# Kernel tuning notes

Hardware: AMD Instinct MI355X
Metric: run time of the kernel (lower is better)

Reference implementation:

```python
import jax, jax.numpy as jnp
import numpy as np
from jax import lax


def setup_inputs() -> dict:
    key = jax.random.key(0)
    ks = jax.random.split(key, 12)
    B, T = 64, 256
    H, EN, ET, D = 512, 256, 256, 256  # hidden, embN, embT, embT_dyn (==ET since embedding_sizeT_dyn=None)
    VN, VT, VS = 300, 1000, 100       # vocab_sizeN, vocab_sizeT, num static ids (static_x_ids = range(100))
    s = 0.05
    ar = jnp.arange(VT)
    inp = {}
    inp["n_input"] = jax.random.randint(ks[0], (B, T), 0, VN)
    inp["t_input"] = jax.random.randint(ks[1], (B, T), 0, VT)
    inp["is_static_vocab"] = ar < VS                      # membership test (t in static_x_ids)
    inp["static2dense"] = jnp.where(ar < VS, ar, 0)       # static id -> row in embeddingT
    inp["dynamic2dense"] = jnp.where(ar >= VS, ar - VS, 0)  # dynamic id -> dense dynamic slot
    inp["embN"] = jax.random.normal(ks[2], (VN, EN)) * s
    inp["embT"] = jax.random.normal(ks[3], (VS, ET)) * s
    inp["W_ih"] = jax.random.normal(ks[4], (4 * H, EN + ET)) * s
    inp["W_hh"] = jax.random.normal(ks[5], (4 * H, H)) * s
    inp["b_ih"] = jax.random.normal(ks[6], (4 * H,)) * s
    inp["b_hh"] = jax.random.normal(ks[7], (4 * H,)) * s
    inp["Wd_ih"] = jax.random.normal(ks[8], (4 * D, EN + H)) * s
    inp["Wd_hh"] = jax.random.normal(ks[9], (4 * D, D)) * s
    inp["bd_ih"] = jax.random.normal(ks[10], (4 * D,)) * s
    inp["bd_hh"] = jax.random.normal(ks[11], (4 * D,)) * s
    inp["hid_init"] = jnp.zeros((H,))
    inp["cell_init"] = jnp.zeros((H,))
    inp["dyn_init_h"] = jnp.zeros((1, D))  # anonym_type='pure_zeros'
    inp["dyn_init_c"] = jnp.zeros((1, D))
    return inp


def _lstm_cell(x, h, c, Wi, Wh, bi, bh):
    # torch.nn.LSTMCell gate order: i, f, g, o
    g = x @ Wi.T + bi + h @ Wh.T + bh
    i, f, gg, o = jnp.split(g, 4, axis=-1)
    c2 = jax.nn.sigmoid(f) * c + jax.nn.sigmoid(i) * jnp.tanh(gg)
    return jax.nn.sigmoid(o) * jnp.tanh(c2), c2


def reference(n_input, t_input, is_static_vocab, static2dense, dynamic2dense,
              embN, embT, W_ih, W_hh, b_ih, b_hh,
              Wd_ih, Wd_hh, bd_ih, bd_hh,
              hid_init, cell_init, dyn_init_h, dyn_init_c):
    # The torch module's growing (lookup_table, de_h, de_c) cache is equivalent to
    # per-(batch, dynamic-token) state arrays Hd/Cd [B, V_dyn, D] with a 'seen' flag:
    # each (b, token) pair owns exactly one cache slot that is read/updated in place.
    B, T = n_input.shape
    H = hid_init.shape[0]
    D = dyn_init_h.shape[-1]
    VD = int(dynamic2dense.max()) + 1  # number of dynamic vocab slots (static at setup)
    bidx = jnp.arange(B)
    init_h = jnp.broadcast_to(dyn_init_h, (B, D))
    init_c = jnp.broadcast_to(dyn_init_c, (B, D))

    def step(carry, xt):
        h, c, seen, Hd, Cd = carry
        nt, tt = xt
        is_st = is_static_vocab[tt]            # [B] bool
        didx = dynamic2dense[tt]               # [B] dynamic slot (garbage 0 for static rows, masked below)
        sn = seen[bidx, didx]                  # was this (b, token) created before?
        hd_prev = jnp.where(sn[:, None], Hd[bidx, didx], init_h)
        cd_prev = jnp.where(sn[:, None], Cd[bidx, didx], init_c)
        n_emb = embN[nt]                       # [B, EN] (dropout=0 -> plain lookup)
        # emb_transform is identity (embedding_sizeT_dyn is None)
        h_tensor = jnp.where(is_st[:, None], embT[static2dense[tt]], hd_prev)  # [B, ET]
        h_new, c_new = _lstm_cell(jnp.concatenate([n_emb, h_tensor], 1), h, c, W_ih, W_hh, b_ih, b_hh)
        # dynamic-embedding LSTM: input is (n_emb, previous main hidden h)
        hd_new, cd_new = _lstm_cell(jnp.concatenate([n_emb, h], 1), hd_prev, cd_prev, Wd_ih, Wd_hh, bd_ih, bd_hh)
        dyn = (~is_st)[:, None]
        Hd = Hd.at[bidx, didx].set(jnp.where(dyn, hd_new, Hd[bidx, didx]))
        Cd = Cd.at[bidx, didx].set(jnp.where(dyn, cd_new, Cd[bidx, didx]))
        seen = seen.at[bidx, didx].set(sn | (~is_st))
        return (h_new, c_new, seen, Hd, Cd), h_new

    h0 = jnp.broadcast_to(hid_init, (B, H)) + 0.0
    c0 = jnp.broadcast_to(cell_init, (B, H)) + 0.0
    carry0 = (h0, c0,
              jnp.zeros((B, VD), dtype=bool),
              jnp.zeros((B, VD, D), dtype=embN.dtype),
              jnp.zeros((B, VD, D), dtype=embN.dtype))
    _, outs = lax.scan(step, carry0, (n_input.T, t_input.T))  # outs: [T, B, H]
    return jnp.transpose(outs, (1, 0, 2))                     # [B, T, H]
```

## Files before the change

### kernel.cpp

```cpp
#include <hip/hip_runtime.h>


typedef _Float16 f16;
typedef _Float16 f16x8 __attribute__((ext_vector_type(8)));
typedef float f32x4 __attribute__((ext_vector_type(4)));

#define B_ 64
#define T_ 256
#define H_ 512
#define EN_ 256
#define ET_ 256
#define D_ 256
#define VN_ 300
#define VS_ 100

#define NB_MAIN_ 128
#define NB_DYN_ 64
#define NBLK_ 192
#define NTHR_ 256
#define NSH_ 64
#define PER_SHARD_ (NBLK_ / NSH_)
#define POLL_CAP_ (1u << 22)

static constexpr size_t OFF_CNT  = 0;
static constexpr size_t OFF_EMBN = 4096;
static constexpr size_t OFF_EMBT = OFF_EMBN + (size_t)VN_ * EN_ * 2;
static constexpr size_t OFF_DINH = OFF_EMBT + (size_t)VS_ * ET_ * 2;
static constexpr size_t OFF_PREV = OFF_DINH + 1024;
static constexpr size_t OFF_HH   = OFF_PREV + (size_t)T_ * B_ * 4;
static constexpr size_t OFF_HD   = OFF_HH + (size_t)(T_ + 1) * B_ * H_ * 2;
static constexpr size_t OFF_CD   = OFF_HD + (size_t)T_ * B_ * D_ * 2;
static constexpr size_t WS_NEED  = OFF_CD + (size_t)T_ * B_ * D_ * 4;

struct RnnParams {
  const int* n_input; const int* t_input; const int* s2d;
  const float* W_ih; const float* W_hh; const float* b_ih; const float* b_hh;
  const float* Wd_ih; const float* Wd_hh; const float* bd_ih; const float* bd_hh;
  const float* cell_init; const float* dyn_init_c;
  const f16* embN16; const f16* embT16; const f16* dynih16;
  const int* prev;
  f16* Hhist; f16* HdHist; float* CdHist;
  float* out; unsigned* cnt;
};

__device__ __forceinline__ float sigm(float x) { return 1.f / (1.f + __expf(-x)); }
__device__ __forceinline__ float tanh_fast(float x) {
  float e = __expf(2.f * x);
  return 1.f - 2.f / (e + 1.f);
}

__device__ __forceinline__ void cstore8(void* p, unsigned long long v) {
  __hip_atomic_store((unsigned long long*)p, v, __ATOMIC_RELAXED,
                     __HIP_MEMORY_SCOPE_AGENT);
}
__device__ __forceinline__ void cstore16(void* p, f32x4 v) {
  asm volatile("global_store_dwordx4 %0, %1, off sc0 sc1"
               :: "v"(p), "v"(v) : "memory");
}
__device__ __forceinline__ float4 scload16f(const float* p) {
  float4 v;
  asm volatile("global_load_dwordx4 %0, %1, off sc0 sc1\n\ts_waitcnt vmcnt(0)"
               : "=&v"(v) : "v"(p) : "memory");
  return v;
}
__device__ __forceinline__ void lds_barrier() {
  asm volatile("s_waitcnt lgkmcnt(0)\n\ts_barrier" ::: "memory");
}

__global__ void setup_kernel(const float* embN, const float* embT,
                             const float* hid_init, const float* dyn_init_h,
                             f16* embN16, f16* embT16, f16* dynih16,
                             f16* Hhist0, unsigned* cnt) {
  int i = blockIdx.x * blockDim.x + threadIdx.x;
  if (i < 1024)      cnt[i] = 0u;
  if (i < VN_ * EN_) embN16[i] = (f16)embN[i];
  if (i < VS_ * ET_) embT16[i] = (f16)embT[i];
  if (i < D_)        dynih16[i] = (f16)dyn_init_h[i];
  if (i < B_ * H_) {
    int b = i >> 9, k = i & 511;
    Hhist0[(k >> 3) * 512 + b * 8 + (k & 7)] = (f16)hid_init[k];
  }
  __threadfence();
}

__global__ void prev_kernel(const int* t_input, const int* s2d, int* prev) {
  int idx = blockIdx.x * blockDim.x + threadIdx.x;
  if (idx < B_ * T_) {
    int b = idx / T_, t = idx % T_;
    int tt = t_input[b * T_ + t];
    int p = -1;
    if (s2d[tt] != tt) {
      for (int q = t - 1; q >= 0; --q)
        if (t_input[b * T_ + q] == tt) { p = q; break; }
    }
    prev[t * B_ + b] = p;
  }
  __threadfence();
}

__device__ __forceinline__ void resolve(const RnnParams& p, bool isDyn, int t, int b,
                                        int tprev,
                                        const f16** aN, const f16** aX,
                                        const float** aC, int* dynw, int* rc) {
  const int nt = p.n_input[b * T_ + t];
  aN[b] = p.embN16 + (size_t)nt * EN_;
  const int tt = p.t_input[b * T_ + t];
  const int pv = p.prev[t * B_ + b];
  rc[b] = (pv >= 0 && pv == tprev) ? 1 : 0;
  const f16* hd = (pv >= 0) ? (p.HdHist + ((size_t)pv * B_ + b) * D_) : p.dynih16;
  const int s2 = p.s2d[tt];
  const bool st = (s2 == tt);
  if (!isDyn) {
    aX[b] = st ? (p.embT16 + (size_t)s2 * ET_) : hd;
  } else {
    aX[b] = hd;
    aC[b] = (pv >= 0) ? (p.CdHist + ((size_t)pv * B_ + b) * D_) : p.dyn_init_c;
    dynw[b] = st ? 0 : 1;
  }
}

__global__ __launch_bounds__(NTHR_, 1) void rnn_main(RnnParams p) {
  const int blk  = blockIdx.x;
  const int tid  = threadIdx.x;
  const int wave = tid >> 6;
  const int lane = tid & 63;
  const bool isDyn = (blk >= NB_MAIN_);
  const int u0 = isDyn ? (blk - NB_MAIN_) * 4 : blk * 4;

  __threadfence();

  __shared__ float s_bias[16];
  __shared__ float s_scr[64][17];
  __shared__ const f16*  s_aN[2][64];
  __shared__ const f16*  s_aX[2][64];
  __shared__ const float* s_aC[2][64];
  __shared__ int s_dynw[2][64];
  __shared__ int s_rc[2][64];

  const int nIdx = lane & 15;
  const int ui = nIdx & 3, gate = nIdx >> 2;
  const int ko = (lane >> 4) * 8;
  f16x8 w[32];
  if (!isDyn) {
    const int r = gate * H_ + u0 + ui;
#pragma unroll
    for (int s = 0; s < 32; ++s) {
      const int k = s * 32 + ko;
      const float* src = (k < 512) ? (p.W_ih + (size_t)r * 512 + k)
                                   : (p.W_hh + (size_t)r * 512 + (k - 512));
      f16x8 v;
#pragma unroll
      for (int j = 0; j < 8; ++j) v[j] = (f16)src[j];
      w[s] = v;
    }
  } else {
    const int r = gate * D_ + u0 + ui;
#pragma unroll
    for (int s = 0; s < 32; ++s) {
      const int k = s * 32 + ko;
      const float* src = (k < 768) ? (p.Wd_ih + (size_t)r * 768 + k)
                                   : (p.Wd_hh + (size_t)r * 256 + (k - 768));
      f16x8 v;
#pragma unroll
      for (int j = 0; j < 8; ++j) v[j] = (f16)src[j];
      w[s] = v;
    }
  }
  if (tid < 16) {
    int g2 = tid >> 2, un2 = tid & 3;
    s_bias[tid] = isDyn ? (p.bd_ih[g2 * D_ + u0 + un2] + p.bd_hh[g2 * D_ + u0 + un2])
                        : (p.b_ih[g2 * H_ + u0 + un2] + p.b_hh[g2 * H_ + u0 + un2]);
  }
  float creg[4] = {0.f, 0.f, 0.f, 0.f};
  if (tid < 64 && !isDyn) {
#pragma unroll
    for (int un = 0; un < 4; ++un) creg[un] = p.cell_init[u0 + un];
  }
  if (tid < 64)
    resolve(p, isDyn, 0, tid, -1, s_aN[0], s_aX[0], s_aC[0], s_dynw[0], s_rc[0]);
  __syncthreads();

  const int b = (wave << 4) + (lane & 15);
  f16x8 pf[16];
  float4 cvp = {0.f, 0.f, 0.f, 0.f};
  {
    const f16* pN = s_aN[0][b];
    const f16* pX = s_aX[0][b];
#pragma unroll
    for (int i = 0; i < 8; ++i) pf[i] = *(const f16x8*)(pN + i * 32 + ko);
#pragma unroll
    for (int i = 0; i < 8; ++i) pf[8 + i] = *(const f16x8*)(pX + i * 32 + ko);
    if (isDyn && tid < 64) cvp = *(const float4*)(s_aC[0][tid] + u0);
  }
  const int hoff = ((lane >> 4) << 9) + ((lane & 15) << 3) + (wave << 7);

  for (int t = 0; t < T_; ++t) {
    const int pb = t & 1;

    const f16* pH2 = p.Hhist + (size_t)t * 32768 + hoff;
    f16x8 hh[16];
#pragma unroll
    for (int i = 0; i < 16; ++i) hh[i] = *(const f16x8*)(pH2 + i * 2048);

    {
      const int need = s_rc[pb][b];
      if (__any(need)) {
        if (need) {
          const f16* pX = s_aX[pb][b];
#pragma unroll
          for (int i = 0; i < 8; ++i)
            asm volatile("global_load_dwordx4 %0, %1, off sc0 sc1"
                         : "=&v"(pf[8 + i]) : "v"(pX + i * 32 + ko));
        }
        asm volatile("s_waitcnt vmcnt(0)" ::: "memory");
        __builtin_amdgcn_sched_barrier(0);
      }
    }

    f32x4 ac[4] = {{0,0,0,0},{0,0,0,0},{0,0,0,0},{0,0,0,0}};
    if (!isDyn) {
#pragma unroll
      for (int i = 0; i < 8; ++i)
        ac[i & 3] = __builtin_amdgcn_mfma_f32_16x16x32_f16(pf[i], w[i], ac[i & 3], 0, 0, 0);
#pragma unroll
      for (int i = 0; i < 8; ++i)
        ac[i & 3] = __builtin_amdgcn_mfma_f32_16x16x32_f16(pf[8 + i], w[8 + i], ac[i & 3], 0, 0, 0);
#pragma unroll
      for (int i = 0; i < 16; ++i)
        ac[i & 3] = __builtin_amdgcn_mfma_f32_16x16x32_f16(hh[i], w[16 + i], ac[i & 3], 0, 0, 0);
    } else {
#pragma unroll
      for (int i = 0; i < 8; ++i)
        ac[i & 3] = __builtin_amdgcn_mfma_f32_16x16x32_f16(pf[i], w[i], ac[i & 3], 0, 0, 0);
#pragma unroll
      for (int i = 0; i < 8; ++i)
        ac[i & 3] = __builtin_amdgcn_mfma_f32_16x16x32_f16(pf[8 + i], w[24 + i], ac[i & 3], 0, 0, 0);
#pragma unroll
      for (int i = 0; i < 16; ++i)
        ac[i & 3] = __builtin_amdgcn_mfma_f32_16x16x32_f16(hh[i], w[8 + i], ac[i & 3], 0, 0, 0);
    }
    f32x4 acc = (ac[0] + ac[1]) + (ac[2] + ac[3]);
#pragma unroll
    for (int j = 0; j < 4; ++j)
      s_scr[(wave << 4) + ((lane >> 4) << 2) + j][lane & 15] = acc[j];
    lds_barrier();

    if (tid < 64) {
      const int eb = tid;
      if (isDyn) {
        const int cneed = s_rc[pb][eb];
        if (__any(cneed)) {
          if (cneed) cvp = scload16f(s_aC[pb][eb] + u0);
          __builtin_amdgcn_sched_barrier(0);
        }
      }
      float g[16];
#pragma unroll
      for (int n = 0; n < 16; ++n) g[n] = s_scr[eb][n] + s_bias[n];
      if (!isDyn) {
        float4 ho;
        union { f16 h[4]; unsigned long long u; } pk;
#pragma unroll
        for (int un = 0; un < 4; ++un) {
          float c = sigm(g[4 + un]) * creg[un] + sigm(g[un]) * tanh_fast(g[8 + un]);
          creg[un] = c;
          float h = sigm(g[12 + un]) * tanh_fast(c);
          (&ho.x)[un] = h;
          pk.h[un] = (f16)h;
        }
        *(float4*)&p.out[((size_t)eb * T_ + t) * H_ + u0] = ho;
        cstore8(&p.Hhist[(size_t)(t + 1) * 32768 + (size_t)(u0 >> 3) * 512
                         + (size_t)eb * 8 + ((u0 >> 2) & 1) * 4], pk.u);
      } else {
        const float cold[4] = {cvp.x, cvp.y, cvp.z, cvp.w};
        f32x4 co;
        union { f16 h[4]; unsigned long long u; } pk;
#pragma unroll
        for (int un = 0; un < 4; ++un) {
          float c = sigm(g[4 + un]) * cold[un] + sigm(g[un]) * tanh_fast(g[8 + un]);
          float h = sigm(g[12 + un]) * tanh_fast(c);
          pk.h[un] = (f16)h;
          co[un] = c;
        }
        if (s_dynw[pb][eb]) {
          cstore8(&p.HdHist[((size_t)t * B_ + eb) * D_ + u0], pk.u);
          cstore16(&p.CdHist[((size_t)t * B_ + eb) * D_ + u0], co);
        }
      }
    } else if (tid < 128 && t + 1 < T_) {
      resolve(p, isDyn, t + 1, tid - 64, t,
              s_aN[pb ^ 1], s_aX[pb ^ 1], s_aC[pb ^ 1], s_dynw[pb ^ 1], s_rc[pb ^ 1]);
    }
    lds_barrier();

    if (t + 1 < T_) {
      if (wave == 0) {
        asm volatile("s_waitcnt vmcnt(0)" ::: "memory");
        if (tid == 0)
          __hip_atomic_fetch_add(&p.cnt[(blk & (NSH_ - 1)) << 4], 1u,
                                 __ATOMIC_RELAXED, __HIP_MEMORY_SCOPE_AGENT);
      }
      {
        const f16* pN2 = s_aN[pb ^ 1][b];
        const f16* pX2 = s_aX[pb ^ 1][b];
#pragma unroll
        for (int i = 0; i < 8; ++i) pf[i] = *(const f16x8*)(pN2 + i * 32 + ko);
#pragma unroll
        for (int i = 0; i < 8; ++i) pf[8 + i] = *(const f16x8*)(pX2 + i * 32 + ko);
        if (isDyn && tid < 64) cvp = *(const float4*)(s_aC[pb ^ 1][tid] + u0);
      }
      if (wave == 1) {
        const unsigned tgt = (unsigned)(t + 1) * PER_SHARD_;
        unsigned it = 0;
        while (__hip_atomic_load(&p.cnt[lane << 4], __ATOMIC_RELAXED,
                                 __HIP_MEMORY_SCOPE_AGENT) < tgt &&
               ++it < POLL_CAP_)
          __builtin_amdgcn_s_sleep(1);
      }
      lds_barrier();
    }
  }
}

extern "C" void kernel_launch(void* const* d_in, const int* in_sizes, int n_in,
                              void* d_out, int out_size, void* d_ws, size_t ws_size,
                              hipStream_t stream) {
  (void)in_sizes; (void)n_in; (void)out_size;
  const int* n_input   = (const int*)d_in[0];
  const int* t_input   = (const int*)d_in[1];
  const int* s2d       = (const int*)d_in[3];
  const float* embN    = (const float*)d_in[5];
  const float* embT    = (const float*)d_in[6];
  const float* W_ih    = (const float*)d_in[7];
  const float* W_hh    = (const float*)d_in[8];
  const float* b_ih    = (const float*)d_in[9];
  const float* b_hh    = (const float*)d_in[10];
  const float* Wd_ih   = (const float*)d_in[11];
  const float* Wd_hh   = (const float*)d_in[12];
  const float* bd_ih   = (const float*)d_in[13];
  const float* bd_hh   = (const float*)d_in[14];
  const float* hid_init  = (const float*)d_in[15];
  const float* cell_init = (const float*)d_in[16];
  const float* dyn_init_h = (const float*)d_in[17];
  const float* dyn_init_c = (const float*)d_in[18];

  char* ws = (char*)d_ws;
  unsigned* cnt  = (unsigned*)(ws + OFF_CNT);
  f16* embN16    = (f16*)(ws + OFF_EMBN);
  f16* embT16    = (f16*)(ws + OFF_EMBT);
  f16* dynih16   = (f16*)(ws + OFF_DINH);
  int* prev      = (int*)(ws + OFF_PREV);
  f16* Hhist     = (f16*)(ws + OFF_HH);
  f16* HdHist    = (f16*)(ws + OFF_HD);
  float* CdHist  = (float*)(ws + OFF_CD);
  if (ws_size < WS_NEED) return;

  setup_kernel<<<dim3((VN_ * EN_ + NTHR_ - 1) / NTHR_), dim3(NTHR_), 0, stream>>>(
      embN, embT, hid_init, dyn_init_h, embN16, embT16, dynih16, Hhist, cnt);
  prev_kernel<<<dim3((B_ * T_ + NTHR_ - 1) / NTHR_), dim3(NTHR_), 0, stream>>>(
      t_input, s2d, prev);

  RnnParams prm;
  prm.n_input = n_input; prm.t_input = t_input; prm.s2d = s2d;
  prm.W_ih = W_ih; prm.W_hh = W_hh; prm.b_ih = b_ih; prm.b_hh = b_hh;
  prm.Wd_ih = Wd_ih; prm.Wd_hh = Wd_hh; prm.bd_ih = bd_ih; prm.bd_hh = bd_hh;
  prm.cell_init = cell_init; prm.dyn_init_c = dyn_init_c;
  prm.embN16 = embN16; prm.embT16 = embT16; prm.dynih16 = dynih16;
  prm.prev = prev; prm.Hhist = Hhist; prm.HdHist = HdHist; prm.CdHist = CdHist;
  prm.out = (float*)d_out; prm.cnt = cnt;

  void* args[] = { &prm };
  hipError_t e = hipLaunchCooperativeKernel((const void*)rnn_main,
                                            dim3(NBLK_), dim3(NTHR_), args, 0, stream);
  if (e != hipSuccess) {
    rnn_main<<<dim3(NBLK_), dim3(NTHR_), 0, stream>>>(prm);
  }
}
```

Baseline: 1.217 ms.

## Replace global grid barrier with split main/dynamic counters and on-demand polling

Drops the per-step all-block barrier. Main and dynamic blocks now bump separate sharded counters, and each wave polls only for what it actually consumes. The main-hidden history is waited on at the start of each step. Dynamic-state loads wait on the dynamic counters only when a recent producer step is involved, which lets dynamic blocks run up to a step behind and overlaps work across steps. This adds more polling from every wave and the risk of subtle ordering bugs, for example reading HdHist before it is written, or the prefetch waiting on t-1.

After: 1.268 ms. 4.2% more time.

```diff
diff --git a/kernel.cpp b/kernel.cpp
--- a/kernel.cpp
+++ b/kernel.cpp
@@ -18,9 +18,9 @@
 #define NB_DYN_ 64
 #define NBLK_ 192
 #define NTHR_ 256
-#define NSH_ 64
-#define PER_SHARD_ (NBLK_ / NSH_)
 #define POLL_CAP_ (1u << 22)
+
+#define DNER_W_ 512
 
 static constexpr size_t OFF_CNT  = 0;
 static constexpr size_t OFF_EMBN = 4096;
@@ -62,6 +62,15 @@
   asm volatile("global_load_dwordx4 %0, %1, off sc0 sc1\n\ts_waitcnt vmcnt(0)"
                : "=&v"(v) : "v"(p) : "memory");
   return v;
+}
+__device__ __forceinline__ void poll_lines(const unsigned* base, int lane, unsigned tgt) {
+  if (tgt == 0) return;
+  const unsigned* w = base + ((lane & 31) << 4);
+  unsigned it = 0;
+  while (__any(__hip_atomic_load(w, __ATOMIC_RELAXED,
+                                 __HIP_MEMORY_SCOPE_AGENT) < tgt) &&
+         ++it < POLL_CAP_)
+    __builtin_amdgcn_s_sleep(1);
 }
 __device__ __forceinline__ void lds_barrier() {
   asm volatile("s_waitcnt lgkmcnt(0)\n\ts_barrier" ::: "memory");
@@ -98,15 +107,14 @@
   __threadfence();
 }
 
-__device__ __forceinline__ void resolve(const RnnParams& p, bool isDyn, int t, int b,
-                                        int tprev,
+__device__ __forceinline__ void resolve(const RnnParams& p, bool isDyn, int s, int b,
                                         const f16** aN, const f16** aX,
                                         const float** aC, int* dynw, int* rc) {
-  const int nt = p.n_input[b * T_ + t];
+  const int nt = p.n_input[b * T_ + s];
   aN[b] = p.embN16 + (size_t)nt * EN_;
-  const int tt = p.t_input[b * T_ + t];
-  const int pv = p.prev[t * B_ + b];
-  rc[b] = (pv >= 0 && pv == tprev) ? 1 : 0;
+  const int tt = p.t_input[b * T_ + s];
+  const int pv = p.prev[s * B_ + b];
+  rc[b] = (pv >= 0 && pv + 2 >= s) ? 1 : 0;
   const f16* hd = (pv >= 0) ? (p.HdHist + ((size_t)pv * B_ + b) * D_) : p.dynih16;
   const int s2 = p.s2d[tt];
   const bool st = (s2 == tt);
@@ -177,7 +185,7 @@
     for (int un = 0; un < 4; ++un) creg[un] = p.cell_init[u0 + un];
   }
   if (tid < 64)
-    resolve(p, isDyn, 0, tid, -1, s_aN[0], s_aX[0], s_aC[0], s_dynw[0], s_rc[0]);
+    resolve(p, isDyn, 0, tid, s_aN[0], s_aX[0], s_aC[0], s_dynw[0], s_rc[0]);
   __syncthreads();
 
   const int b = (wave << 4) + (lane & 15);
@@ -197,6 +205,8 @@
   for (int t = 0; t < T_; ++t) {
     const int pb = t & 1;
 
+    poll_lines(p.cnt, lane, 4u * (unsigned)t);
+
     const f16* pH2 = p.Hhist + (size_t)t * 32768 + hoff;
     f16x8 hh[16];
 #pragma unroll
@@ -205,6 +215,7 @@
     {
       const int need = s_rc[pb][b];
       if (__any(need)) {
+        poll_lines(p.cnt + DNER_W_, lane, 2u * (unsigned)t);
         if (need) {
           const f16* pX = s_aX[pb][b];
 #pragma unroll
@@ -250,6 +261,7 @@
       if (isDyn) {
         const int cneed = s_rc[pb][eb];
         if (__any(cneed)) {
+          poll_lines(p.cnt + DNER_W_, lane, 2u * (unsigned)t);
           if (cneed) cvp = scload16f(s_aC[pb][eb] + u0);
           __builtin_amdgcn_sched_barrier(0);
         }
@@ -288,7 +300,7 @@
         }
       }
     } else if (tid < 128 && t + 1 < T_) {
-      resolve(p, isDyn, t + 1, tid - 64, t,
+      resolve(p, isDyn, t + 1, tid - 64,
               s_aN[pb ^ 1], s_aX[pb ^ 1], s_aC[pb ^ 1], s_dynw[pb ^ 1], s_rc[pb ^ 1]);
     }
     lds_barrier();
@@ -296,10 +308,15 @@
     if (t + 1 < T_) {
       if (wave == 0) {
         asm volatile("s_waitcnt vmcnt(0)" ::: "memory");
-        if (tid == 0)
-          __hip_atomic_fetch_add(&p.cnt[(blk & (NSH_ - 1)) << 4], 1u,
-                                 __ATOMIC_RELAXED, __HIP_MEMORY_SCOPE_AGENT);
-      }
+        if (lane == 0) {
+          const unsigned wd = isDyn
+              ? (unsigned)(DNER_W_ + (((blk - NB_MAIN_) & 31) << 4))
+              : (unsigned)((blk & 31) << 4);
+          __hip_atomic_fetch_add(&p.cnt[wd], 1u, __ATOMIC_RELAXED,
+                                 __HIP_MEMORY_SCOPE_AGENT);
+        }
+      }
+      poll_lines(p.cnt + DNER_W_, lane, t >= 2 ? 2u * (unsigned)(t - 1) : 0u);
       {
         const f16* pN2 = s_aN[pb ^ 1][b];
         const f16* pX2 = s_aX[pb ^ 1][b];
@@ -309,15 +326,6 @@
         for (int i = 0; i < 8; ++i) pf[8 + i] = *(const f16x8*)(pX2 + i * 32 + ko);
         if (isDyn && tid < 64) cvp = *(const float4*)(s_aC[pb ^ 1][tid] + u0);
       }
-      if (wave == 1) {
-        const unsigned tgt = (unsigned)(t + 1) * PER_SHARD_;
-        unsigned it = 0;
-        while (__hip_atomic_load(&p.cnt[lane << 4], __ATOMIC_RELAXED,
-                                 __HIP_MEMORY_SCOPE_AGENT) < tgt &&
-               ++it < POLL_CAP_)
-          __builtin_amdgcn_s_sleep(1);
-      }
-      lds_barrier();
     }
   }
 }
```
